# Performance work log

Hardware: AMD Instinct MI355X
Metric: run time of the kernel (lower is better)

The kernel has to match this reference:

```python
import jax, jax.numpy as jnp
import numpy as np

B, K, D = 8, 4000, 256
H, DQ, DV = 8, 32, 32
WIN, PAD = 200, 50
STEP = WIN - 2 * PAD  # 100
BETA = 0.25


def setup_inputs() -> dict:
    key = jax.random.key(0)
    ks = jax.random.split(key, 14)
    s = 0.02
    return {
        "query": jax.random.normal(ks[0], (B, K, D), jnp.float32),
        "key": jax.random.normal(ks[1], (B, K, D), jnp.float32),
        "value": jax.random.normal(ks[2], (B, K, D), jnp.float32),
        "Wq": jax.random.normal(ks[3], (D, H * DQ), jnp.float32) * s,
        "bq": jax.random.normal(ks[4], (H * DQ,), jnp.float32) * s,
        "Wk": jax.random.normal(ks[5], (D, H * DQ), jnp.float32) * s,
        "bk": jax.random.normal(ks[6], (H * DQ,), jnp.float32) * s,
        "Wv": jax.random.normal(ks[7], (D, H * DV), jnp.float32) * s,
        "bv": jax.random.normal(ks[8], (H * DV,), jnp.float32) * s,
        "Wo": jax.random.normal(ks[9], (H * DV, D), jnp.float32) * s,
        "bo": jax.random.normal(ks[10], (D,), jnp.float32) * s,
    }


def _windows(x, n_win):
    starts = jnp.arange(n_win) * STEP
    idx = starts[:, None] + jnp.arange(WIN)[None, :]
    return x[:, :, idx, :]


def reference(query, key, value, Wq, bq, Wk, bk, Wv, bv, Wo, bo):
    b, k_len, d = query.shape
    pad = lambda t: jnp.pad(t, ((0, 0), (PAD, PAD), (0, 0)), mode='edge')  # replicate pad
    qp, kp, vp = pad(query), pad(key), pad(value)
    kpad = k_len + 2 * PAD
    n_win = (kpad - WIN) // STEP + 1

    def proj(x, Wm, bias, dh):
        y = x @ Wm + bias                       # [B, Kp, H*dh]
        return y.reshape(b, kpad, H, dh).transpose(0, 2, 1, 3)  # [B, H, Kp, dh]

    q = _windows(proj(qp, Wq, bq, DQ), n_win)
    kk = _windows(proj(kp, Wk, bk, DQ), n_win)
    v = _windows(proj(vp, Wv, bv, DV), n_win)

    scores = jnp.einsum('bhnid,bhnjd->bhnij', q, kk) / jnp.sqrt(jnp.float32(WIN))
    dist = jnp.abs(jnp.arange(WIN)[:, None] - jnp.arange(WIN)[None, :]).astype(scores.dtype)
    cauchy = (1.0 / (1.0 + BETA * dist * dist)) * (1.0 - jnp.eye(WIN, dtype=scores.dtype))
    scores = scores * cauchy
    causal = jnp.triu(jnp.ones((WIN, WIN), dtype=bool), k=1)  # attention_size is not None -> causal masking
    scores = jnp.where(causal, -jnp.inf, scores)
    attn = jax.nn.softmax(scores, axis=-1)
    out = jnp.einsum('bhnij,bhnjd->bhnid', attn, v)
    out = out[:, :, :, PAD:WIN - PAD, :].reshape(b, H, k_len, DV)
    out = out.transpose(0, 2, 1, 3).reshape(b, k_len, H * DV)  # heads concatenated, head-major slices
    return out @ Wo + bo
```

## Files before the change

kernel.cpp:

```cpp
#include <hip/hip_runtime.h>


typedef __bf16 bf16_t;
typedef __bf16 bf16x8 __attribute__((ext_vector_type(8)));
typedef float  f32x4  __attribute__((ext_vector_type(4)));

#define MFMA16(a, b, c) __builtin_amdgcn_mfma_f32_16x16x32_bf16((a), (b), (c), 0, 0, 0)

static __device__ __forceinline__ bf16x8 cvt8(float4 a, float4 b) {
  bf16x8 r;
  r[0] = (bf16_t)a.x; r[1] = (bf16_t)a.y; r[2] = (bf16_t)a.z; r[3] = (bf16_t)a.w;
  r[4] = (bf16_t)b.x; r[5] = (bf16_t)b.y; r[6] = (bf16_t)b.z; r[7] = (bf16_t)b.w;
  return r;
}

static __device__ __forceinline__ unsigned short bbits(bf16_t v) {
  union { bf16_t b; unsigned short u; } c; c.b = v; return c.u;
}

__global__ __launch_bounds__(256)
void prep_weights(const float* __restrict__ Wq, const float* __restrict__ Wk,
                  const float* __restrict__ Wv, const float* __restrict__ Wo,
                  bf16_t* __restrict__ wt) {
  const int mat  = blockIdx.x >> 6;
  const int tile = blockIdx.x & 63;
  const int kt = (tile >> 3) * 32, nt = (tile & 7) * 32;
  const float* W = (mat == 0) ? Wq : (mat == 1) ? Wk : (mat == 2) ? Wv : Wo;
  __shared__ float t[32][33];
  const int tx = threadIdx.x & 31, ty = threadIdx.x >> 5;
#pragma unroll
  for (int i = 0; i < 32; i += 8)
    t[ty + i][tx] = W[(size_t)(kt + ty + i) * 256 + nt + tx];
  __syncthreads();
  bf16_t* dst = wt + (size_t)mat * 65536;
#pragma unroll
  for (int i = 0; i < 32; i += 8)
    dst[(size_t)(nt + ty + i) * 256 + kt + tx] = (bf16_t)t[tx][ty + i];
}

template <int MODE>
__global__ __launch_bounds__(256)
void gemm256(const void* __restrict__ Xv, const bf16_t* __restrict__ Wt,
             const float* __restrict__ bias, void* __restrict__ Out, int M,
             float oscale) {
  constexpr bool INB = (MODE == 3);
  const int m0 = blockIdx.x * 128;
  const int n0 = blockIdx.y * 128;
  __shared__ bf16_t la[128 * 40];
  __shared__ bf16_t lb[128 * 40];
  const int tid  = threadIdx.x;
  const int lane = tid & 63;
  const int wr   = ((tid >> 7) & 1) * 64;
  const int wc   = ((tid >> 6) & 1) * 64;
  const int lo   = lane & 15, hi = lane >> 4;
  const int arow = tid >> 1;
  const int acol = (tid & 1) * 16;
  int ar = m0 + arow; if (ar >= M) ar = M - 1;

  f32x4 acc[4][4] = {};

  for (int kk = 0; kk < 256; kk += 32) {
    if constexpr (!INB) {
      const float* X = (const float*)Xv + (size_t)ar * 256 + kk + acol;
      float4 x0 = ((const float4*)X)[0];
      float4 x1 = ((const float4*)X)[1];
      float4 x2 = ((const float4*)X)[2];
      float4 x3 = ((const float4*)X)[3];
      *(bf16x8*)&la[arow * 40 + acol]     = cvt8(x0, x1);
      *(bf16x8*)&la[arow * 40 + acol + 8] = cvt8(x2, x3);
    } else {
      const bf16_t* X = (const bf16_t*)Xv + (size_t)ar * 256 + kk + acol;
      *(bf16x8*)&la[arow * 40 + acol]     = ((const bf16x8*)X)[0];
      *(bf16x8*)&la[arow * 40 + acol + 8] = ((const bf16x8*)X)[1];
    }
    {
      const bf16_t* Wp = Wt + (size_t)(n0 + arow) * 256 + kk + acol;
      *(bf16x8*)&lb[arow * 40 + acol]     = ((const bf16x8*)Wp)[0];
      *(bf16x8*)&lb[arow * 40 + acol + 8] = ((const bf16x8*)Wp)[1];
    }
    __syncthreads();

    bf16x8 af[4], bfv[4];
#pragma unroll
    for (int mi = 0; mi < 4; ++mi)
      af[mi] = *(const bf16x8*)&la[(wr + mi * 16 + lo) * 40 + hi * 8];
#pragma unroll
    for (int ni = 0; ni < 4; ++ni)
      bfv[ni] = *(const bf16x8*)&lb[(wc + ni * 16 + lo) * 40 + hi * 8];
#pragma unroll
    for (int mi = 0; mi < 4; ++mi)
#pragma unroll
      for (int ni = 0; ni < 4; ++ni)
        acc[mi][ni] = MFMA16(af[mi], bfv[ni], acc[mi][ni]);
    __syncthreads();
  }

#pragma unroll
  for (int mi = 0; mi < 4; ++mi)
#pragma unroll
    for (int ni = 0; ni < 4; ++ni) {
      const int n   = n0 + wc + ni * 16 + lo;
      const float bia = bias[n];
      const int mb  = m0 + wr + mi * 16 + hi * 4;
      if (mb >= M) continue;
      if constexpr (MODE == 0) {
        bf16_t* O = (bf16_t*)Out;
#pragma unroll
        for (int r = 0; r < 4; ++r)
          O[(size_t)(mb + r) * 256 + n] = (bf16_t)((acc[mi][ni][r] + bia) * oscale);
      } else if constexpr (MODE == 1) {
        const int b = mb / 4000, t = mb - b * 4000;
        bf16_t* O = (bf16_t*)Out;
#pragma unroll
        for (int r = 0; r < 4; ++r)
          O[((size_t)b * 4064 + t + 50 + r) * 256 + n] = (bf16_t)(acc[mi][ni][r] + bia);
      } else if constexpr (MODE == 2) {
        const int b = mb / 4000, t = mb - b * 4000;
        const int h = n >> 5, dv = n & 31;
        bf16_t* O = (bf16_t*)Out + ((size_t)((b * 8 + h) * 32 + dv)) * 4064 + t + 50;
        unsigned short e0 = bbits((bf16_t)(acc[mi][ni][0] + bia));
        unsigned short e1 = bbits((bf16_t)(acc[mi][ni][1] + bia));
        unsigned short e2 = bbits((bf16_t)(acc[mi][ni][2] + bia));
        unsigned short e3 = bbits((bf16_t)(acc[mi][ni][3] + bia));
        unsigned* O32 = (unsigned*)O;
        O32[0] = (unsigned)e0 | ((unsigned)e1 << 16);
        O32[1] = (unsigned)e2 | ((unsigned)e3 << 16);
      } else {
        float* O = (float*)Out;
#pragma unroll
        for (int r = 0; r < 4; ++r)
          O[(size_t)(mb + r) * 256 + n] = acc[mi][ni][r] + bia;
      }
    }
}

__global__ void fill_edges(bf16_t* __restrict__ kb, bf16_t* __restrict__ vt, int nb) {
  const int idx = blockIdx.x * 256 + threadIdx.x;
  const int kcnt = nb * 64 * 256;
  if (idx < kcnt) {
    const int b  = idx >> 14;
    const int pp = (idx >> 8) & 63;
    const int nn = idx & 255;
    const int p  = (pp < 50) ? pp : pp + 4000;
    bf16_t v = (pp < 50) ? kb[((size_t)b * 4064 + 50) * 256 + nn] : (bf16_t)0.f;
    kb[((size_t)b * 4064 + p) * 256 + nn] = v;
  } else {
    const int j  = idx - kcnt;
    const int bh = j >> 11;
    const int dv = (j >> 6) & 31;
    const int pp = j & 63;
    const int p  = (pp < 50) ? pp : pp + 4000;
    bf16_t v = (pp < 50) ? vt[((size_t)bh * 32 + dv) * 4064 + 50] : (bf16_t)0.f;
    vt[((size_t)bh * 32 + dv) * 4064 + p] = v;
  }
}

__global__ __launch_bounds__(448)
void attn_win(const bf16_t* __restrict__ qb, const bf16_t* __restrict__ kb,
              const bf16_t* __restrict__ vt, bf16_t* __restrict__ ao) {
  const int blk = blockIdx.x;
  const int n = blk % 40;
  const int h = (blk / 40) & 7;
  const int b = blk / 320;
  const int wv = threadIdx.x >> 6;
  const int lane = threadIdx.x & 63;
  const int lo = lane & 15, hi = lane >> 4;

  __shared__ __align__(16) bf16_t E[7][16][168];

  const int i0 = 50 + 16 * wv;
  int jtmax = (65 + 16 * wv) >> 4;
  if (jtmax > 9) jtmax = 9;

  int tq = n * 100 + 16 * wv + lo;
  if (tq > 3999) tq = 3999;
  const bf16x8 qf = *(const bf16x8*)&qb[((size_t)b * 4000 + tq) * 256 + h * 32 + hi * 8];

  const f32x4 zero = {0.f, 0.f, 0.f, 0.f};

  const int dbase = i0 + hi * 4 - lo;
  for (int jt = 0; jt <= jtmax; ++jt) {
    const bf16x8 kf = *(const bf16x8*)&kb[((size_t)(b * 4064 + n * 100 + jt * 16 + lo)) * 256 + h * 32 + hi * 8];
    const f32x4 s = MFMA16(qf, kf, zero);
#pragma unroll
    for (int r = 0; r < 4; ++r) {
      const int d = dbase + r - jt * 16;
      const float df = (float)d;
      float c = __builtin_amdgcn_rcpf(__builtin_fmaf(0.25f * df, df, 1.f));
      c = (d == 0) ? 0.f : c;
      float e = __expf(s[r] * c);
      e = (d < 0) ? 0.f : e;
      E[wv][hi * 4 + r][jt * 16 + lo] = (bf16_t)e;
    }
  }
  for (int jt = jtmax + 1; jt < 10; ++jt) {
#pragma unroll
    for (int r = 0; r < 4; ++r)
      E[wv][hi * 4 + r][jt * 16 + lo] = (bf16_t)0.f;
  }

  bf16x8 onesf;
#pragma unroll
  for (int u = 0; u < 8; ++u) onesf[u] = (bf16_t)1.0f;

  f32x4 o0 = zero, o1 = zero, sm = zero;
  const size_t vbase = ((size_t)((b * 8 + h) * 32)) * 4064 + n * 100;
  const int reach = jtmax * 16 + 16;
#pragma unroll
  for (int kt = 0; kt < 5; ++kt) if (kt * 32 < reach) {
    const bf16x8 pf = *(const bf16x8*)&E[wv][lo][kt * 32 + hi * 8];
    const bf16x8 v0 = *(const bf16x8*)&vt[vbase + (size_t)lo * 4064 + kt * 32 + hi * 8];
    const bf16x8 v1 = *(const bf16x8*)&vt[vbase + (size_t)(16 + lo) * 4064 + kt * 32 + hi * 8];
    o0 = MFMA16(pf, v0, o0);
    o1 = MFMA16(pf, v1, o1);
    sm = MFMA16(pf, onesf, sm);
  }

#pragma unroll
  for (int r = 0; r < 4; ++r) {
    const int i = i0 + hi * 4 + r;
    if (i < 150) {
      const float ri = __builtin_amdgcn_rcpf(sm[r]);
      const int t = n * 100 + i - 50;
      bf16_t* op = &ao[((size_t)b * 4000 + t) * 256 + h * 32];
      op[lo]      = (bf16_t)(o0[r] * ri);
      op[16 + lo] = (bf16_t)(o1[r] * ri);
    }
  }
}

extern "C" void kernel_launch(void* const* d_in, const int* in_sizes, int n_in,
                              void* d_out, int out_size, void* d_ws, size_t ws_size,
                              hipStream_t stream) {
  (void)in_sizes; (void)n_in; (void)out_size;
  const float* query = (const float*)d_in[0];
  const float* key   = (const float*)d_in[1];
  const float* value = (const float*)d_in[2];
  const float* Wq = (const float*)d_in[3];
  const float* bq = (const float*)d_in[4];
  const float* Wk = (const float*)d_in[5];
  const float* bk = (const float*)d_in[6];
  const float* Wv = (const float*)d_in[7];
  const float* bv = (const float*)d_in[8];
  const float* Wo = (const float*)d_in[9];
  const float* bo = (const float*)d_in[10];

  int bc = 8;
  while (bc > 1 && 524288ull + (unsigned long long)bc * 8257536ull > (unsigned long long)ws_size)
    bc >>= 1;

  bf16_t* wt = (bf16_t*)d_ws;
  bf16_t* qb = wt + 4 * 65536;
  bf16_t* kb = qb + (size_t)bc * 4000 * 256;
  bf16_t* vt = kb + (size_t)bc * 4064 * 256;
  bf16_t* ao = vt + (size_t)bc * 8 * 32 * 4064;

  prep_weights<<<256, 256, 0, stream>>>(Wq, Wk, Wv, Wo, wt);

  const float qscale = 0.07071067811865475f;

  for (int b0 = 0; b0 < 8; b0 += bc) {
    const int M = bc * 4000;
    const int mblk = (M + 127) / 128;
    const float* qx = query + (size_t)b0 * 4000 * 256;
    const float* kx = key   + (size_t)b0 * 4000 * 256;
    const float* vx = value + (size_t)b0 * 4000 * 256;
    float* ox = (float*)d_out + (size_t)b0 * 4000 * 256;

    gemm256<0><<<dim3(mblk, 2), 256, 0, stream>>>(qx, wt + 0 * 65536, bq, qb, M, qscale);
    gemm256<1><<<dim3(mblk, 2), 256, 0, stream>>>(kx, wt + 1 * 65536, bk, kb, M, 1.f);
    gemm256<2><<<dim3(mblk, 2), 256, 0, stream>>>(vx, wt + 2 * 65536, bv, vt, M, 1.f);
    fill_edges<<<bc * 128, 256, 0, stream>>>(kb, vt, bc);
    attn_win<<<bc * 320, 448, 0, stream>>>(qb, kb, vt, ao);
    gemm256<3><<<dim3(mblk, 2), 256, 0, stream>>>(ao, wt + 3 * 65536, bo, ox, M, 1.f);
  }
}
```

Before: 112.5 us.

## Retile projection GEMMs to full-width N and interleave score/PV in attention

The projection GEMMs switch from 128x128 tiles with 256 threads to 64-row tiles spanning all 256 output columns with 512 threads. Each input row is now read and converted once instead of twice across N-blocks, and the grid has more blocks in M. The attention kernel computes exp-scores per 32-column chunk right before the PV MFMA, which shrinks the shared E buffer from 168 to 40 columns and removes the separate zero-fill pass. The trade-off is fewer MFMAs per LDS load in the GEMM (1 A-fragment per 8 B-fragments) and shorter per-wave work, which may cut latency hiding.

After: 106.2 us. 5.7% less time.

```diff
diff --git a/kernel.cpp b/kernel.cpp
--- a/kernel.cpp
+++ b/kernel.cpp
@@ -2,15 +2,15 @@
 
 
 typedef __bf16 bf16_t;
+typedef __bf16 bf16x4 __attribute__((ext_vector_type(4)));
 typedef __bf16 bf16x8 __attribute__((ext_vector_type(8)));
 typedef float  f32x4  __attribute__((ext_vector_type(4)));
 
 #define MFMA16(a, b, c) __builtin_amdgcn_mfma_f32_16x16x32_bf16((a), (b), (c), 0, 0, 0)
 
-static __device__ __forceinline__ bf16x8 cvt8(float4 a, float4 b) {
-  bf16x8 r;
+static __device__ __forceinline__ bf16x4 cvt4(float4 a) {
+  bf16x4 r;
   r[0] = (bf16_t)a.x; r[1] = (bf16_t)a.y; r[2] = (bf16_t)a.z; r[3] = (bf16_t)a.w;
-  r[4] = (bf16_t)b.x; r[5] = (bf16_t)b.y; r[6] = (bf16_t)b.z; r[7] = (bf16_t)b.w;
   return r;
 }
 
@@ -39,99 +39,84 @@
 }
 
 template <int MODE>
-__global__ __launch_bounds__(256)
+__global__ __launch_bounds__(512)
 void gemm256(const void* __restrict__ Xv, const bf16_t* __restrict__ Wt,
              const float* __restrict__ bias, void* __restrict__ Out, int M,
-             float oscale) {
+             float oscale = 1.f) {
   constexpr bool INB = (MODE == 3);
-  const int m0 = blockIdx.x * 128;
-  const int n0 = blockIdx.y * 128;
-  __shared__ bf16_t la[128 * 40];
-  __shared__ bf16_t lb[128 * 40];
+  const int m0 = blockIdx.x * 64;
+  __shared__ bf16_t la[64 * 40];
+  __shared__ bf16_t lb[256 * 40];
   const int tid  = threadIdx.x;
   const int lane = tid & 63;
-  const int wr   = ((tid >> 7) & 1) * 64;
-  const int wc   = ((tid >> 6) & 1) * 64;
+  const int wv   = tid >> 6;
+  const int wm   = (wv & 3) * 16;
+  const int wn   = (wv >> 2) * 128;
   const int lo   = lane & 15, hi = lane >> 4;
-  const int arow = tid >> 1;
-  const int acol = (tid & 1) * 16;
-  int ar = m0 + arow; if (ar >= M) ar = M - 1;
-
-  f32x4 acc[4][4] = {};
+  int ar = m0 + (tid >> 3); if (ar >= M) ar = M - 1;
+
+  f32x4 acc[8] = {};
 
   for (int kk = 0; kk < 256; kk += 32) {
     if constexpr (!INB) {
-      const float* X = (const float*)Xv + (size_t)ar * 256 + kk + acol;
-      float4 x0 = ((const float4*)X)[0];
-      float4 x1 = ((const float4*)X)[1];
-      float4 x2 = ((const float4*)X)[2];
-      float4 x3 = ((const float4*)X)[3];
-      *(bf16x8*)&la[arow * 40 + acol]     = cvt8(x0, x1);
-      *(bf16x8*)&la[arow * 40 + acol + 8] = cvt8(x2, x3);
+      const float* X = (const float*)Xv + (size_t)ar * 256 + kk + (tid & 7) * 4;
+      *(bf16x4*)&la[(tid >> 3) * 40 + (tid & 7) * 4] = cvt4(*(const float4*)X);
     } else {
-      const bf16_t* X = (const bf16_t*)Xv + (size_t)ar * 256 + kk + acol;
-      *(bf16x8*)&la[arow * 40 + acol]     = ((const bf16x8*)X)[0];
-      *(bf16x8*)&la[arow * 40 + acol + 8] = ((const bf16x8*)X)[1];
+      const bf16_t* X = (const bf16_t*)Xv + (size_t)ar * 256 + kk + (tid & 7) * 4;
+      *(bf16x4*)&la[(tid >> 3) * 40 + (tid & 7) * 4] = *(const bf16x4*)X;
     }
     {
-      const bf16_t* Wp = Wt + (size_t)(n0 + arow) * 256 + kk + acol;
-      *(bf16x8*)&lb[arow * 40 + acol]     = ((const bf16x8*)Wp)[0];
-      *(bf16x8*)&lb[arow * 40 + acol + 8] = ((const bf16x8*)Wp)[1];
+      const bf16_t* Wp = Wt + (size_t)(tid >> 1) * 256 + kk + (tid & 1) * 16;
+      bf16_t* dst = &lb[(tid >> 1) * 40 + (tid & 1) * 16];
+      *(bf16x8*)dst       = ((const bf16x8*)Wp)[0];
+      *(bf16x8*)(dst + 8) = ((const bf16x8*)Wp)[1];
     }
     __syncthreads();
 
-    bf16x8 af[4], bfv[4];
-#pragma unroll
-    for (int mi = 0; mi < 4; ++mi)
-      af[mi] = *(const bf16x8*)&la[(wr + mi * 16 + lo) * 40 + hi * 8];
-#pragma unroll
-    for (int ni = 0; ni < 4; ++ni)
-      bfv[ni] = *(const bf16x8*)&lb[(wc + ni * 16 + lo) * 40 + hi * 8];
-#pragma unroll
-    for (int mi = 0; mi < 4; ++mi)
-#pragma unroll
-      for (int ni = 0; ni < 4; ++ni)
-        acc[mi][ni] = MFMA16(af[mi], bfv[ni], acc[mi][ni]);
+    const bf16x8 af = *(const bf16x8*)&la[(wm + lo) * 40 + hi * 8];
+#pragma unroll
+    for (int ni = 0; ni < 8; ++ni) {
+      const bf16x8 bfv = *(const bf16x8*)&lb[(wn + ni * 16 + lo) * 40 + hi * 8];
+      acc[ni] = MFMA16(af, bfv, acc[ni]);
+    }
     __syncthreads();
   }
 
 #pragma unroll
-  for (int mi = 0; mi < 4; ++mi)
-#pragma unroll
-    for (int ni = 0; ni < 4; ++ni) {
-      const int n   = n0 + wc + ni * 16 + lo;
-      const float bia = bias[n];
-      const int mb  = m0 + wr + mi * 16 + hi * 4;
-      if (mb >= M) continue;
-      if constexpr (MODE == 0) {
-        bf16_t* O = (bf16_t*)Out;
-#pragma unroll
-        for (int r = 0; r < 4; ++r)
-          O[(size_t)(mb + r) * 256 + n] = (bf16_t)((acc[mi][ni][r] + bia) * oscale);
-      } else if constexpr (MODE == 1) {
-        const int b = mb / 4000, t = mb - b * 4000;
-        bf16_t* O = (bf16_t*)Out;
-#pragma unroll
-        for (int r = 0; r < 4; ++r)
-          O[((size_t)b * 4064 + t + 50 + r) * 256 + n] = (bf16_t)(acc[mi][ni][r] + bia);
-      } else if constexpr (MODE == 2) {
-        const int b = mb / 4000, t = mb - b * 4000;
-        const int h = n >> 5, dv = n & 31;
-        bf16_t* O = (bf16_t*)Out + ((size_t)((b * 8 + h) * 32 + dv)) * 4064 + t + 50;
-        unsigned short e0 = bbits((bf16_t)(acc[mi][ni][0] + bia));
-        unsigned short e1 = bbits((bf16_t)(acc[mi][ni][1] + bia));
-        unsigned short e2 = bbits((bf16_t)(acc[mi][ni][2] + bia));
-        unsigned short e3 = bbits((bf16_t)(acc[mi][ni][3] + bia));
-        unsigned* O32 = (unsigned*)O;
-        O32[0] = (unsigned)e0 | ((unsigned)e1 << 16);
-        O32[1] = (unsigned)e2 | ((unsigned)e3 << 16);
-      } else {
-        float* O = (float*)Out;
-#pragma unroll
-        for (int r = 0; r < 4; ++r)
-          O[(size_t)(mb + r) * 256 + n] = acc[mi][ni][r] + bia;
-      }
-    }
+  for (int ni = 0; ni < 8; ++ni) {
+    const int n   = wn + ni * 16 + lo;
+    const float bia = bias[n];
+    const int mb  = m0 + wm + hi * 4;
+    if (mb >= M) continue;
+    if constexpr (MODE == 0) {
+      bf16_t* O = (bf16_t*)Out;
+#pragma unroll
+      for (int r = 0; r < 4; ++r)
+        O[(size_t)(mb + r) * 256 + n] = (bf16_t)((acc[ni][r] + bia) * oscale);
+    } else if constexpr (MODE == 1) {
+      const int b = mb / 4000, t = mb - b * 4000;
+      bf16_t* O = (bf16_t*)Out;
+#pragma unroll
+      for (int r = 0; r < 4; ++r)
+        O[((size_t)b * 4064 + t + 50 + r) * 256 + n] = (bf16_t)(acc[ni][r] + bia);
+    } else if constexpr (MODE == 2) {
+      const int b = mb / 4000, t = mb - b * 4000;
+      const int h = n >> 5, dv = n & 31;
+      bf16_t* O = (bf16_t*)Out + ((size_t)((b * 8 + h) * 32 + dv)) * 4064 + t + 50;
+      unsigned short e0 = bbits((bf16_t)(acc[ni][0] + bia));
+      unsigned short e1 = bbits((bf16_t)(acc[ni][1] + bia));
+      unsigned short e2 = bbits((bf16_t)(acc[ni][2] + bia));
+      unsigned short e3 = bbits((bf16_t)(acc[ni][3] + bia));
+      unsigned* O32 = (unsigned*)O;
+      O32[0] = (unsigned)e0 | ((unsigned)e1 << 16);
+      O32[1] = (unsigned)e2 | ((unsigned)e3 << 16);
+    } else {
+      float* O = (float*)Out;
+#pragma unroll
+      for (int r = 0; r < 4; ++r)
+        O[(size_t)(mb + r) * 256 + n] = acc[ni][r] + bia;
+    }
+  }
 }
 
 __global__ void fill_edges(bf16_t* __restrict__ kb, bf16_t* __restrict__ vt, int nb) {
@@ -166,49 +151,52 @@
   const int lane = threadIdx.x & 63;
   const int lo = lane & 15, hi = lane >> 4;
 
-  __shared__ __align__(16) bf16_t E[7][16][168];
+  __shared__ __align__(16) bf16_t E[7][16][40];
 
   const int i0 = 50 + 16 * wv;
   int jtmax = (65 + 16 * wv) >> 4;
   if (jtmax > 9) jtmax = 9;
+  const int reach = jtmax * 16 + 16;
 
   int tq = n * 100 + 16 * wv + lo;
   if (tq > 3999) tq = 3999;
   const bf16x8 qf = *(const bf16x8*)&qb[((size_t)b * 4000 + tq) * 256 + h * 32 + hi * 8];
 
   const f32x4 zero = {0.f, 0.f, 0.f, 0.f};
-
-  const int dbase = i0 + hi * 4 - lo;
-  for (int jt = 0; jt <= jtmax; ++jt) {
-    const bf16x8 kf = *(const bf16x8*)&kb[((size_t)(b * 4064 + n * 100 + jt * 16 + lo)) * 256 + h * 32 + hi * 8];
-    const f32x4 s = MFMA16(qf, kf, zero);
-#pragma unroll
-    for (int r = 0; r < 4; ++r) {
-      const int d = dbase + r - jt * 16;
-      const float df = (float)d;
-      float c = __builtin_amdgcn_rcpf(__builtin_fmaf(0.25f * df, df, 1.f));
-      c = (d == 0) ? 0.f : c;
-      float e = __expf(s[r] * c);
-      e = (d < 0) ? 0.f : e;
-      E[wv][hi * 4 + r][jt * 16 + lo] = (bf16_t)e;
-    }
-  }
-  for (int jt = jtmax + 1; jt < 10; ++jt) {
-#pragma unroll
-    for (int r = 0; r < 4; ++r)
-      E[wv][hi * 4 + r][jt * 16 + lo] = (bf16_t)0.f;
-  }
-
   bf16x8 onesf;
 #pragma unroll
   for (int u = 0; u < 8; ++u) onesf[u] = (bf16_t)1.0f;
 
   f32x4 o0 = zero, o1 = zero, sm = zero;
   const size_t vbase = ((size_t)((b * 8 + h) * 32)) * 4064 + n * 100;
-  const int reach = jtmax * 16 + 16;
+  const size_t kbase = ((size_t)(b * 4064 + n * 100)) * 256 + h * 32 + hi * 8;
+  const int dbase = i0 + hi * 4 - lo;
+
 #pragma unroll
   for (int kt = 0; kt < 5; ++kt) if (kt * 32 < reach) {
-    const bf16x8 pf = *(const bf16x8*)&E[wv][lo][kt * 32 + hi * 8];
+#pragma unroll
+    for (int half = 0; half < 2; ++half) {
+      const int jt = kt * 2 + half;
+      if (jt <= jtmax) {
+        const bf16x8 kf = *(const bf16x8*)&kb[kbase + (size_t)(jt * 16 + lo) * 256];
+        const f32x4 s = MFMA16(qf, kf, zero);
+#pragma unroll
+        for (int r = 0; r < 4; ++r) {
+          const int d = dbase + r - jt * 16;
+          const float df = (float)d;
+          float c = __builtin_amdgcn_rcpf(__builtin_fmaf(0.25f * df, df, 1.f));
+          c = (d == 0) ? 0.f : c;
+          float e = __expf(s[r] * c);
+          e = (d < 0) ? 0.f : e;
+          E[wv][hi * 4 + r][half * 16 + lo] = (bf16_t)e;
+        }
+      } else {
+#pragma unroll
+        for (int r = 0; r < 4; ++r)
+          E[wv][hi * 4 + r][half * 16 + lo] = (bf16_t)0.f;
+      }
+    }
+    const bf16x8 pf = *(const bf16x8*)&E[wv][lo][hi * 8];
     const bf16x8 v0 = *(const bf16x8*)&vt[vbase + (size_t)lo * 4064 + kt * 32 + hi * 8];
     const bf16x8 v1 = *(const bf16x8*)&vt[vbase + (size_t)(16 + lo) * 4064 + kt * 32 + hi * 8];
     o0 = MFMA16(pf, v0, o0);
@@ -261,17 +249,17 @@
 
   for (int b0 = 0; b0 < 8; b0 += bc) {
     const int M = bc * 4000;
-    const int mblk = (M + 127) / 128;
+    const int mblk = (M + 63) / 64;
     const float* qx = query + (size_t)b0 * 4000 * 256;
     const float* kx = key   + (size_t)b0 * 4000 * 256;
     const float* vx = value + (size_t)b0 * 4000 * 256;
     float* ox = (float*)d_out + (size_t)b0 * 4000 * 256;
 
-    gemm256<0><<<dim3(mblk, 2), 256, 0, stream>>>(qx, wt + 0 * 65536, bq, qb, M, qscale);
-    gemm256<1><<<dim3(mblk, 2), 256, 0, stream>>>(kx, wt + 1 * 65536, bk, kb, M, 1.f);
-    gemm256<2><<<dim3(mblk, 2), 256, 0, stream>>>(vx, wt + 2 * 65536, bv, vt, M, 1.f);
+    gemm256<0><<<dim3(mblk), 512, 0, stream>>>(qx, wt + 0 * 65536, bq, qb, M, qscale);
+    gemm256<1><<<dim3(mblk), 512, 0, stream>>>(kx, wt + 1 * 65536, bk, kb, M, 1.f);
+    gemm256<2><<<dim3(mblk), 512, 0, stream>>>(vx, wt + 2 * 65536, bv, vt, M, 1.f);
     fill_edges<<<bc * 128, 256, 0, stream>>>(kb, vt, bc);
     attn_win<<<bc * 320, 448, 0, stream>>>(qb, kb, vt, ao);
-    gemm256<3><<<dim3(mblk, 2), 256, 0, stream>>>(ao, wt + 3 * 65536, bo, ox, M, 1.f);
-  }
-}
+    gemm256<3><<<dim3(mblk), 512, 0, stream>>>(ao, wt + 3 * 65536, bo, ox, M, 1.f);
+  }
+}
```
